# Kernel tuning notes

Measured on AMD Instinct MI355X. Metric: run time of the kernel, lower is better.

Reference implementation:

```python
import jax, jax.numpy as jnp
import numpy as np
from jax import lax

EPS = 1e-20

def _conv(x, w, b):
    # stride-2 conv, padding=1, NCHW/OIHW (torch Conv2d semantics)
    y = lax.conv_general_dilated(x, w, (2, 2), ((1, 1), (1, 1)),
                                 dimension_numbers=('NCHW', 'OIHW', 'NCHW'))
    return y + b[None, :, None, None]

def _deconv(x, w, b):
    # ConvTranspose2d(k=4, s=2, p=1): doubles spatial dims (== SAME transpose padding)
    y = lax.conv_transpose(x, w, (2, 2), 'SAME',
                           dimension_numbers=('NCHW', 'OIHW', 'NCHW'))
    return y + b[None, :, None, None]

def _enc_switch(h, win, bin_, wout, bout, wsw, bsw, gnoise):
    r = jax.nn.relu(h)
    hid = jnp.einsum('bd,kds->bks', r, win) + bin_            # [B,K,S]
    y_logits = jnp.einsum('bks,ks->bk', hid, wsw) + bsw       # [B,K]
    g = -jnp.log(gnoise + EPS)                                # Gumbel noise
    y_soft = jax.nn.softmax(y_logits + g, axis=1)
    y_index = jnp.argmax(y_soft, axis=1)                      # [B]
    one_hot = jax.nn.one_hot(y_index, y_logits.shape[1], dtype=y_soft.dtype)
    y_hard = one_hot - lax.stop_gradient(y_soft) + y_soft     # straight-through
    outs = jnp.einsum('bks,ksd->bkd', hid, wout) + bout       # [B,K,192]
    out = jnp.take_along_axis(outs, y_index[:, None, None], axis=1)[:, 0]
    gate = jnp.take_along_axis(y_hard, y_index[:, None], axis=1)  # [B,1] (training gate)
    return h + out * gate, y_logits, y_index, y_hard

def _dec_switch(h, win, bin_, wout, bout, y_index, y_hard):
    r = jax.nn.relu(h)
    hid = jnp.einsum('bd,kds->bks', r, win) + bin_
    outs = jnp.einsum('bks,ksd->bkd', hid, wout) + bout
    out = jnp.take_along_axis(outs, y_index[:, None, None], axis=1)[:, 0]
    gate = jnp.take_along_axis(y_hard, y_index[:, None], axis=1)
    return h + out * gate

def setup_inputs() -> dict:
    key = jax.random.key(0)
    B, C, L, D, K, S = 1024, 3, 10, 192, 10, 10
    ks = jax.random.split(key, 48)
    def n(i, shape, s=0.05):
        return jax.random.normal(ks[i], shape, jnp.float32) * s
    return {
        'x': jax.random.uniform(ks[0], (B, C, 64, 64), jnp.float32),
        'gnoise': jax.random.exponential(ks[1], (L, B, K)).astype(jnp.float32),
        'znoise': jax.random.normal(ks[2], (B, L), jnp.float32),
        'cw1': n(3, (32, C, 4, 4)), 'cb1': n(4, (32,)),
        'cw2': n(5, (32, 32, 4, 4)), 'cb2': n(6, (32,)),
        'cw3': n(7, (64, 32, 4, 4)), 'cb3': n(8, (64,)),
        'cw4': n(9, (64, 64, 4, 4)), 'cb4': n(10, (64,)),
        'fc_w': n(11, (1024, D)), 'fc_b': n(12, (D,)),
        'ein_w': n(13, (L, K, D, S)), 'ein_b': n(14, (L, K, S)),
        'eout_w': n(15, (L, K, S, D)), 'eout_b': n(16, (L, K, D)),
        'esw_w': n(17, (L, K, S)), 'esw_b': n(18, (L, K)),
        'mean_w': n(19, (D, L)), 'mean_b': n(20, (L,)),
        'lv_w': n(21, (D, L)), 'lv_b': n(22, (L,)),
        'fcl_w': n(23, (L, D)), 'fcl_b': n(24, (D,)),
        'din_w': n(25, (L, K, D, S)), 'din_b': n(26, (L, K, S)),
        'dout_w': n(27, (L, K, S, D)), 'dout_b': n(28, (L, K, D)),
        'dfc_w': n(29, (D, 1024)), 'dfc_b': n(30, (1024,)),
        'dw1': n(31, (64, 64, 4, 4)), 'db1': n(32, (64,)),
        'dw2': n(33, (32, 64, 4, 4)), 'db2': n(34, (32,)),
        'dw3': n(35, (32, 32, 4, 4)), 'db3': n(36, (32,)),
        'dw4': n(37, (C, 32, 4, 4)), 'db4': n(38, (C,)),
    }

def reference(x, gnoise, znoise, cw1, cb1, cw2, cb2, cw3, cb3, cw4, cb4,
              fc_w, fc_b, ein_w, ein_b, eout_w, eout_b, esw_w, esw_b,
              mean_w, mean_b, lv_w, lv_b, fcl_w, fcl_b,
              din_w, din_b, dout_w, dout_b, dfc_w, dfc_b,
              dw1, db1, dw2, db2, dw3, db3, dw4, db4):
    # ---- encoder convs ----
    h = jax.nn.relu(_conv(x, cw1, cb1))
    h = jax.nn.relu(_conv(h, cw2, cb2))
    h = jax.nn.relu(_conv(h, cw3, cb3))
    h = jax.nn.relu(_conv(h, cw4, cb4))           # [B,64,4,4]
    h = h.reshape(-1, 1024) @ fc_w + fc_b         # [B,192]
    # ---- encoder FC switches (sequential over latents) ----
    L = ein_w.shape[0]
    ys_index, ys_hard = [], []
    for i in range(L):
        h, _, yi, yh = _enc_switch(h, ein_w[i], ein_b[i], eout_w[i], eout_b[i],
                                   esw_w[i], esw_b[i], gnoise[i])
        ys_index.append(yi); ys_hard.append(yh)
    r = jax.nn.relu(h)
    z_mean = r @ mean_w + mean_b
    z_logvar = r @ lv_w + lv_b
    # ---- reparameterize ----
    z = znoise * jnp.exp(z_logvar / 2) + z_mean
    # ---- decoder ----
    d = z @ fcl_w + fcl_b
    for i in range(L):
        d = _dec_switch(d, din_w[i], din_b[i], dout_w[i], dout_b[i],
                        ys_index[i], ys_hard[i])
    d = jax.nn.relu(d)
    d = jax.nn.relu(d @ dfc_w + dfc_b)
    d = d.reshape(-1, 64, 4, 4)
    d = jax.nn.relu(_deconv(d, dw1, db1))
    d = jax.nn.relu(_deconv(d, dw2, db2))
    d = jax.nn.relu(_deconv(d, dw3, db3))
    recon_x = _deconv(d, dw4, db4)                # [B,C,64,64] logits
    return recon_x, z, z_mean, z_logvar
```

## Files before the change

kernel.cpp:

```cpp
#include <hip/hip_runtime.h>
#include <hip/hip_bf16.h>
#include <math.h>


#define BATCH 1024

using short8  = __attribute__((ext_vector_type(8))) short;
using f32x4   = __attribute__((ext_vector_type(4))) float;
using ushort4v = __attribute__((ext_vector_type(4))) ushort;

__device__ __forceinline__ ushort f2bf(float f) {
    uint u = __float_as_uint(f);
    uint r = (u + 0x7fffu + ((u >> 16) & 1u)) >> 16;
    return (ushort)r;
}
__device__ __forceinline__ float bf2f(ushort u) {
    return __uint_as_float(((uint)u) << 16);
}

__device__ __forceinline__ void conv_frag_elem(const float* __restrict__ w,
                                               ushort* __restrict__ frag,
                                               int idx, int CIN, int COUT) {
    int NCH = CIN / 32, NT = COUT / 16;
    int j = idx & 7; int lane = (idx >> 3) & 63; int rest = idx >> 9;
    int ntile = rest % NT; rest /= NT;
    int ch = rest % NCH; int tap = rest / NCH;
    int o = ntile * 16 + (lane & 15);
    int i = ch * 32 + (lane >> 4) * 8 + j;
    frag[idx] = f2bf(w[((size_t)(o * CIN + i)) * 16 + tap]);
}
__device__ __forceinline__ void deconv_frag_elem(const float* __restrict__ w,
                                                 ushort* __restrict__ frag,
                                                 int idx, int CIN, int COUT) {
    int NCH = CIN / 32, NT = COUT / 16;
    int j = idx & 7; int lane = (idx >> 3) & 63; int rest = idx >> 9;
    int ntile = rest % NT; rest /= NT;
    int ch = rest % NCH; rest /= NCH;
    int tapidx = rest % 4; int cls = rest / 4;
    int py = cls >> 1, px = cls & 1, a = tapidx >> 1, b = tapidx & 1;
    int tap = (py + 2 * a) * 4 + (px + 2 * b);
    int o = ntile * 16 + (lane & 15);
    int i = ch * 32 + (lane >> 4) * 8 + j;
    frag[idx] = f2bf(w[((size_t)(o * CIN + i)) * 16 + tap]);
}

__global__ __launch_bounds__(256)
void prep_all(const float* __restrict__ cw1, const float* __restrict__ cw2,
              const float* __restrict__ cw3, const float* __restrict__ cw4,
              const float* __restrict__ dw1, const float* __restrict__ dw2,
              const float* __restrict__ dw3, const float* __restrict__ dw4,
              const float* __restrict__ ein_w, const float* __restrict__ fc_w,
              const float* __restrict__ dfc_w, const float* __restrict__ x,
              ushort* __restrict__ c1g, ushort* __restrict__ c2g,
              ushort* __restrict__ c3g, ushort* __restrict__ c4g,
              ushort* __restrict__ d1g, ushort* __restrict__ d2g,
              ushort* __restrict__ d3g, ushort* __restrict__ d4g,
              ushort* __restrict__ encwTb, ushort* __restrict__ fc1g,
              ushort* __restrict__ dfcg, ushort* __restrict__ xh) {
    const int b = blockIdx.x, t = threadIdx.x;
    if (b < 8) {
        int idx = b * 256 + t;
        if (idx < 2048) {
            int j = idx & 7; int lane = (idx >> 3) & 63;
            int ntile = (idx >> 9) & 1; int s = idx >> 10;
            int o = ntile * 16 + (lane & 15);
            int kg = lane >> 4;
            int tap = s * 8 + kg * 2 + (j >> 2);
            int c = j & 3;
            c1g[idx] = (c < 3) ? f2bf(cw1[((size_t)(o * 3 + c)) * 16 + tap]) : (ushort)0;
        }
    } else if (b < 72) {
        conv_frag_elem(cw2, c2g, (b - 8) * 256 + t, 32, 32);
    } else if (b < 200) {
        conv_frag_elem(cw3, c3g, (b - 72) * 256 + t, 32, 64);
    } else if (b < 456) {
        conv_frag_elem(cw4, c4g, (b - 200) * 256 + t, 64, 64);
    } else if (b < 712) {
        deconv_frag_elem(dw1, d1g, (b - 456) * 256 + t, 64, 64);
    } else if (b < 840) {
        deconv_frag_elem(dw2, d2g, (b - 712) * 256 + t, 64, 32);
    } else if (b < 904) {
        deconv_frag_elem(dw3, d3g, (b - 840) * 256 + t, 32, 32);
    } else if (b < 936) {
        int idx = (b - 904) * 256 + t;
        if (idx < 4608) {
            int jj = idx & 7; int lane = (idx >> 3) & 63; int nbi = idx >> 9;
            int dy = nbi / 3, dx = nbi % 3;
            int j = lane & 15;
            int k = (lane >> 4) * 8 + jj;
            int cls = j >> 2, och = j & 3;
            int py = cls >> 1, px = cls & 1;
            int a2 = dy - py, b2 = dx - px;
            ushort v = 0;
            if (och < 3 && (unsigned)a2 < 2u && (unsigned)b2 < 2u) {
                int tap = (py + 2 * a2) * 4 + (px + 2 * b2);
                v = f2bf(dw4[((size_t)(och * 32 + k)) * 16 + tap]);
            }
            d4g[idx] = v;
        }
    } else if (b < 1686) {
        int idx = (b - 936) * 256 + t;
        if (idx < 192000) {
            int ks = idx % 100;
            int d = (idx / 100) % 192;
            int l = idx / 19200;
            int k = ks / 10, s = ks % 10;
            encwTb[idx] = f2bf(ein_w[(size_t)l * 19200 + k * 1920 + d * 10 + s]);
        }
    } else if (b < 2454) {
        int idx = (b - 1686) * 256 + t;
        int jj = idx & 7; int lane = (idx >> 3) & 63; int rest = idx >> 9;
        int nt = rest % 12, s = rest / 12;
        int k_nat = s * 32 + (lane >> 4) * 8 + jj;
        int d = (k_nat & 63) * 16 + (k_nat >> 6);
        int j = nt * 16 + (lane & 15);
        fc1g[idx] = f2bf(fc_w[(size_t)d * 192 + j]);
    } else if (b < 3222) {
        int idx = (b - 2454) * 256 + t;
        int jj = idx & 7; int lane = (idx >> 3) & 63; int rest = idx >> 9;
        int nt = rest % 64, s = rest / 64;
        int k = s * 32 + (lane >> 4) * 8 + jj;
        int j_nat = nt * 16 + (lane & 15);
        int d = (j_nat & 63) * 16 + (j_nat >> 6);
        dfcg[idx] = f2bf(dfc_w[(size_t)k * 1024 + d]);
    } else {
        const int n = b - 3222;
        const float* xb = x + (size_t)n * 12288;
        ushort* ob = xh + ((size_t)n << 14);
        #pragma unroll
        for (int i = 0; i < 4; ++i) {
            const int p0 = (i * 256 + t) << 2;
            const float4 v0 = *(const float4*)(xb + p0);
            const float4 v1 = *(const float4*)(xb + 4096 + p0);
            const float4 v2 = *(const float4*)(xb + 8192 + p0);
            short8 o0, o1;
            o0[0] = (short)f2bf(v0.x); o0[1] = (short)f2bf(v1.x); o0[2] = (short)f2bf(v2.x); o0[3] = 0;
            o0[4] = (short)f2bf(v0.y); o0[5] = (short)f2bf(v1.y); o0[6] = (short)f2bf(v2.y); o0[7] = 0;
            o1[0] = (short)f2bf(v0.z); o1[1] = (short)f2bf(v1.z); o1[2] = (short)f2bf(v2.z); o1[3] = 0;
            o1[4] = (short)f2bf(v0.w); o1[5] = (short)f2bf(v1.w); o1[6] = (short)f2bf(v2.w); o1[7] = 0;
            *(short8*)(ob + (size_t)(p0 << 2)) = o0;
            *(short8*)(ob + (size_t)(p0 << 2) + 8) = o1;
        }
    }
}

__global__ __launch_bounds__(512)
void conv12_fused(const ushort* __restrict__ xh, const ushort* __restrict__ w1frag,
                  const float* __restrict__ b1, const ushort* __restrict__ w2frag,
                  const float* __restrict__ b2, ushort* __restrict__ out) {
    __shared__ ushort mid[576 * 40];
    const int t = threadIdx.x;
    const int lane = t & 63, w = t >> 6;
    const int m = lane & 15, kg = lane >> 4;
    const int h = blockIdx.x & 1, n = blockIdx.x >> 1;
    const int base = 16 * h - 1;
    const ushort* xb = xh + ((size_t)n << 14);

    short8 bf1[4];
    #pragma unroll
    for (int f = 0; f < 4; ++f)
        bf1[f] = *(const short8*)(w1frag + (f << 9) + lane * 8);

    auto gatherA = [&](int mt, short8* av) {
        const int lp = mt * 16 + m;
        const int lx = lp & 31, lyy = lp >> 5;
        const int my = base + lyy;
        const int iy0 = 2 * my - 1, ix0 = 2 * lx - 1;
        #pragma unroll
        for (int s = 0; s < 2; ++s) {
            union { ushort4v h4[2]; short8 s8; } a;
            #pragma unroll
            for (int tt = 0; tt < 2; ++tt) {
                const int tap = s * 8 + kg * 2 + tt;
                const int ky = tap >> 2, kx = tap & 3;
                const int iy = iy0 + ky, ix = ix0 + kx;
                ushort4v v = {0, 0, 0, 0};
                if ((unsigned)iy < 64u && (unsigned)ix < 64u)
                    v = *(const ushort4v*)(xb + (size_t)(((iy << 6) + ix) << 2));
                a.h4[tt] = v;
            }
            av[s] = a.s8;
        }
    };
    auto commitA = [&](int mt, short8* av) {
        f32x4 acc[2] = {{0,0,0,0},{0,0,0,0}};
        #pragma unroll
        for (int s = 0; s < 2; ++s)
            #pragma unroll
            for (int nt = 0; nt < 2; ++nt)
                acc[nt] = __builtin_amdgcn_mfma_f32_16x16x32_bf16(av[s], bf1[s * 2 + nt], acc[nt], 0, 0, 0);
        #pragma unroll
        for (int nt = 0; nt < 2; ++nt) {
            const int och = (nt << 4) + m;
            const float bv = b1[och];
            #pragma unroll
            for (int r = 0; r < 4; ++r) {
                const int lpr = (mt << 4) + (kg << 2) + r;
                mid[(size_t)lpr * 40 + och] = f2bf(fmaxf(acc[nt][r] + bv, 0.f));
            }
        }
    };

    {
        short8 avA[2], avB[2];
        gatherA(w, avA);
        gatherA(w + 8, avB);
        commitA(w, avA);
        commitA(w + 8, avB);
        gatherA(w + 16, avA);
        gatherA(w + 24, avB);
        commitA(w + 16, avA);
        commitA(w + 24, avB);
        if (w < 4) {
            gatherA(w + 32, avA);
            commitA(w + 32, avA);
        }
    }
    __syncthreads();
    for (int it = 0; it < 2; ++it) {
        const int u = it * 8 + w;
        const int nt = u & 1, mt2 = u >> 1;
        const int p2 = (mt2 << 4) + m;
        const int ox2 = p2 & 15, ly2 = p2 >> 4;
        const int oy2 = 8 * h + ly2;
        const int iy0 = 2 * oy2 - 1, ix0 = 2 * ox2 - 1;
        f32x4 acc = {0, 0, 0, 0};
        const ushort* wl = w2frag + ((size_t)nt << 9) + lane * 8;
        #pragma unroll
        for (int ky = 0; ky < 4; ++ky) {
            const int iy = iy0 + ky;
            const bool vy = (unsigned)iy < 32u;
            const int liy = iy - base;
            #pragma unroll
            for (int kx = 0; kx < 4; ++kx) {
                const int ix = ix0 + kx;
                const bool v = vy && ((unsigned)ix < 32u);
                short8 a = {0, 0, 0, 0, 0, 0, 0, 0};
                if (v) a = *(const short8*)(mid + (size_t)((liy << 5) + ix) * 40 + kg * 8);
                const short8 b = *(const short8*)(wl + ((size_t)((ky * 4 + kx) * 2) << 9));
                acc = __builtin_amdgcn_mfma_f32_16x16x32_bf16(a, b, acc, 0, 0, 0);
            }
        }
        const int och = (nt << 4) + m;
        const float bv = b2[och];
        ushort* ob = out + ((size_t)n * 256 + 128 * h + (mt2 << 4) + (kg << 2)) * 32;
        #pragma unroll
        for (int r = 0; r < 4; ++r)
            ob[r * 32 + och] = f2bf(fmaxf(acc[r] + bv, 0.f));
    }
}

__global__ __launch_bounds__(256)
void conv34_fused(const ushort* __restrict__ in, const ushort* __restrict__ w3frag,
                  const float* __restrict__ b3, const ushort* __restrict__ w4frag,
                  const float* __restrict__ b4, ushort* __restrict__ out) {
    __shared__ ushort mid[64 * 64];
    const int t = threadIdx.x;
    const int lane = t & 63, w = t >> 6;
    const int m = lane & 15, kg = lane >> 4;
    const int n = blockIdx.x;
    const ushort* ibase = in + ((size_t)n << 13);

    {
        const int p = (w << 4) + m;
        const int ox = p & 7, oy = p >> 3;
        const int iy0 = 2 * oy - 1, ix0 = 2 * ox - 1;
        f32x4 acc[4] = {{0,0,0,0},{0,0,0,0},{0,0,0,0},{0,0,0,0}};
        #pragma unroll
        for (int ky = 0; ky < 4; ++ky) {
            const int iy = iy0 + ky;
            const bool vy = (unsigned)iy < 16u;
            #pragma unroll
            for (int kx = 0; kx < 4; ++kx) {
                const int ix = ix0 + kx;
                const bool v = vy && ((unsigned)ix < 16u);
                short8 a = {0, 0, 0, 0, 0, 0, 0, 0};
                if (v) a = *(const short8*)(ibase + (size_t)((iy << 4) + ix) * 32 + kg * 8);
                const int tap = ky * 4 + kx;
                #pragma unroll
                for (int nt = 0; nt < 4; ++nt) {
                    const short8 b = *(const short8*)(w3frag + ((size_t)(tap * 4 + nt) << 9) + lane * 8);
                    acc[nt] = __builtin_amdgcn_mfma_f32_16x16x32_bf16(a, b, acc[nt], 0, 0, 0);
                }
            }
        }
        #pragma unroll
        for (int nt = 0; nt < 4; ++nt) {
            const int och = (nt << 4) + m;
            const float bv = b3[och];
            #pragma unroll
            for (int r = 0; r < 4; ++r) {
                const int pr = (w << 4) + (kg << 2) + r;
                mid[(size_t)pr * 64 + och] = f2bf(fmaxf(acc[nt][r] + bv, 0.f));
            }
        }
    }
    __syncthreads();
    {
        const int ox = m & 3, oy = m >> 2;
        const int iy0 = 2 * oy - 1, ix0 = 2 * ox - 1;
        f32x4 acc = {0, 0, 0, 0};
        const ushort* wl = w4frag + ((size_t)w << 9) + lane * 8;
        #pragma unroll
        for (int ky = 0; ky < 4; ++ky) {
            const int iy = iy0 + ky;
            const bool vy = (unsigned)iy < 8u;
            #pragma unroll
            for (int kx = 0; kx < 4; ++kx) {
                const int ix = ix0 + kx;
                const bool v = vy && ((unsigned)ix < 8u);
                const int tap = ky * 4 + kx;
                #pragma unroll
                for (int ch = 0; ch < 2; ++ch) {
                    short8 a = {0, 0, 0, 0, 0, 0, 0, 0};
                    if (v) a = *(const short8*)(mid + (size_t)((iy << 3) + ix) * 64 + ch * 32 + kg * 8);
                    const short8 b = *(const short8*)(wl + ((size_t)((tap * 2 + ch) * 4) << 9));
                    acc = __builtin_amdgcn_mfma_f32_16x16x32_bf16(a, b, acc, 0, 0, 0);
                }
            }
        }
        const int och = (w << 4) + m;
        const float bv = b4[och];
        #pragma unroll
        for (int r = 0; r < 4; ++r)
            out[((size_t)n * 16 + (kg << 2) + r) * 64 + och] = f2bf(fmaxf(acc[r] + bv, 0.f));
    }
}

__global__ __launch_bounds__(256)
void deconv12_fused(const ushort* __restrict__ in, const ushort* __restrict__ w1frag,
                    const float* __restrict__ b1, const ushort* __restrict__ w2frag,
                    const float* __restrict__ b2, ushort* __restrict__ out) {
    __shared__ ushort mid[64 * 64];
    const int t = threadIdx.x;
    const int lane = t & 63, w = t >> 6;
    const int m = lane & 15, kg = lane >> 4;
    const int n = blockIdx.x;
    const ushort* ibase = in + ((size_t)n << 10);

    {
        const int oxh = m & 3, oyh = m >> 2;
        f32x4 acc[4] = {{0,0,0,0},{0,0,0,0},{0,0,0,0},{0,0,0,0}};
        const ushort* wl = w1frag + ((size_t)w << 9) + lane * 8;
        #pragma unroll
        for (int ch = 0; ch < 2; ++ch) {
            short8 nb[3][3];
            #pragma unroll
            for (int dy = 0; dy < 3; ++dy) {
                const int iy = oyh + dy - 1;
                const bool vy = (unsigned)iy < 4u;
                #pragma unroll
                for (int dx = 0; dx < 3; ++dx) {
                    const int ix = oxh + dx - 1;
                    short8 a = {0, 0, 0, 0, 0, 0, 0, 0};
                    if (vy && (unsigned)ix < 4u)
                        a = *(const short8*)(ibase + (size_t)((iy << 2) + ix) * 64 + ch * 32 + kg * 8);
                    nb[dy][dx] = a;
                }
            }
            #pragma unroll
            for (int cls = 0; cls < 4; ++cls) {
                const int py = cls >> 1, px = cls & 1;
                #pragma unroll
                for (int ti = 0; ti < 4; ++ti) {
                    const int a2 = ti >> 1, b2i = ti & 1;
                    const short8 b = *(const short8*)(wl + ((size_t)(((cls * 4 + ti) * 2 + ch) * 4) << 9));
                    acc[cls] = __builtin_amdgcn_mfma_f32_16x16x32_bf16(nb[py + a2][px + b2i], b, acc[cls], 0, 0, 0);
                }
            }
        }
        const int och = (w << 4) + m;
        const float bv = b1[och];
        #pragma unroll
        for (int cls = 0; cls < 4; ++cls) {
            const int py = cls >> 1, px = cls & 1;
            #pragma unroll
            for (int r = 0; r < 4; ++r) {
                const int qq = (kg << 2) + r;
                const int oxh2 = qq & 3, oyh2 = qq >> 2;
                const int oy = 2 * oyh2 + py, ox = 2 * oxh2 + px;
                mid[(size_t)((oy << 3) + ox) * 64 + och] = f2bf(fmaxf(acc[cls][r] + bv, 0.f));
            }
        }
    }
    __syncthreads();
    for (int u = w; u < 8; u += 4) {
        const int nt = u & 1, mt = u >> 1;
        const int q = (mt << 4) + m;
        const int oxh = q & 7, oyh = q >> 3;
        f32x4 acc[4] = {{0,0,0,0},{0,0,0,0},{0,0,0,0},{0,0,0,0}};
        const ushort* wl = w2frag + ((size_t)nt << 9) + lane * 8;
        #pragma unroll
        for (int ch = 0; ch < 2; ++ch) {
            short8 nb[3][3];
            #pragma unroll
            for (int dy = 0; dy < 3; ++dy) {
                const int iy = oyh + dy - 1;
                const bool vy = (unsigned)iy < 8u;
                #pragma unroll
                for (int dx = 0; dx < 3; ++dx) {
                    const int ix = oxh + dx - 1;
                    short8 a = {0, 0, 0, 0, 0, 0, 0, 0};
                    if (vy && (unsigned)ix < 8u)
                        a = *(const short8*)(mid + (size_t)((iy << 3) + ix) * 64 + ch * 32 + kg * 8);
                    nb[dy][dx] = a;
                }
            }
            #pragma unroll
            for (int cls = 0; cls < 4; ++cls) {
                const int py = cls >> 1, px = cls & 1;
                #pragma unroll
                for (int ti = 0; ti < 4; ++ti) {
                    const int a2 = ti >> 1, b2i = ti & 1;
                    const short8 b = *(const short8*)(wl + ((size_t)(((cls * 4 + ti) * 2 + ch) * 2) << 9));
                    acc[cls] = __builtin_amdgcn_mfma_f32_16x16x32_bf16(nb[py + a2][px + b2i], b, acc[cls], 0, 0, 0);
                }
            }
        }
        const int och = (nt << 4) + m;
        const float bv = b2[och];
        #pragma unroll
        for (int cls = 0; cls < 4; ++cls) {
            const int py = cls >> 1, px = cls & 1;
            #pragma unroll
            for (int r = 0; r < 4; ++r) {
                const int qq = (mt << 4) + (kg << 2) + r;
                const int oxh2 = qq & 7, oyh2 = qq >> 3;
                const int oy = 2 * oyh2 + py, ox = 2 * oxh2 + px;
                out[((size_t)(n * 16 + oy) * 16 + ox) * 32 + och] = f2bf(fmaxf(acc[cls][r] + bv, 0.f));
            }
        }
    }
}

__global__ __launch_bounds__(256)
void deconv34_fused(const ushort* __restrict__ in, const ushort* __restrict__ w3frag,
                    const float* __restrict__ b3, const ushort* __restrict__ w4frag,
                    const float* __restrict__ b4, float* __restrict__ out) {
    __shared__ ushort mid[20 * 32 * 32];
    const int t = threadIdx.x;
    const int lane = t & 63, w = t >> 6;
    const int m = lane & 15, kg = lane >> 4;
    const int h = blockIdx.x & 1, n = blockIdx.x >> 1;
    const int base = 16 * h - 2;
    const ushort* ibase = in + ((size_t)n << 13);

    for (int u = w; u < 20; u += 4) {
        const int nt = u & 1, mt = u >> 1;
        const int ir = 8 * h - 1 + mt;
        short8 nb[3][3];
        #pragma unroll
        for (int dy = 0; dy < 3; ++dy) {
            const int iy = ir + dy - 1;
            const bool vy = (unsigned)iy < 16u;
            #pragma unroll
            for (int dx = 0; dx < 3; ++dx) {
                const int ix = m + dx - 1;
                short8 a = {0, 0, 0, 0, 0, 0, 0, 0};
                if (vy && (unsigned)ix < 16u)
                    a = *(const short8*)(ibase + (size_t)((iy << 4) + ix) * 32 + kg * 8);
                nb[dy][dx] = a;
            }
        }
        const ushort* wl = w3frag + ((size_t)nt << 9) + lane * 8;
        f32x4 acc[4] = {{0,0,0,0},{0,0,0,0},{0,0,0,0},{0,0,0,0}};
        #pragma unroll
        for (int cls = 0; cls < 4; ++cls) {
            const int py = cls >> 1, px = cls & 1;
            #pragma unroll
            for (int ti = 0; ti < 4; ++ti) {
                const int a2 = ti >> 1, b2 = ti & 1;
                const short8 b = *(const short8*)(wl + ((size_t)((cls * 4 + ti) * 2) << 9));
                acc[cls] = __builtin_amdgcn_mfma_f32_16x16x32_bf16(nb[py + a2][px + b2], b, acc[cls], 0, 0, 0);
            }
        }
        const int och = (nt << 4) + m;
        const int ochSw = och ^ (kg << 3);
        const float bv = b3[och];
        #pragma unroll
        for (int cls = 0; cls < 4; ++cls) {
            const int py = cls >> 1, px = cls & 1;
            const int ly = 2 * mt + py;
            #pragma unroll
            for (int r = 0; r < 4; ++r) {
                const int ox = ((kg << 3) + 2 * r) + px;
                mid[(size_t)((ly << 5) + ox) * 32 + ochSw] = f2bf(fmaxf(acc[cls][r] + bv, 0.f));
            }
        }
    }
    __syncthreads();
    const int clsB = m >> 2, ochB = m & 3;
    const int pyB = clsB >> 1, pxB = clsB & 1;
    for (int it = 0; it < 8; ++it) {
        const int mt2 = it * 4 + w;
        const int oyh = 16 * h + (mt2 >> 1);
        const int oxh = ((mt2 & 1) << 4) + m;
        short8 nb[3][3];
        #pragma unroll
        for (int dy = 0; dy < 3; ++dy) {
            const int iy = oyh + dy - 1;
            const bool vy = (unsigned)iy < 32u;
            const int ly = iy - base;
            #pragma unroll
            for (int dx = 0; dx < 3; ++dx) {
                const int ix = oxh + dx - 1;
                short8 a = {0, 0, 0, 0, 0, 0, 0, 0};
                if (vy && (unsigned)ix < 32u) {
                    const int rb = (kg ^ ((ix >> 3) & 3)) << 3;
                    a = *(const short8*)(mid + (size_t)((ly << 5) + ix) * 32 + rb);
                }
                nb[dy][dx] = a;
            }
        }
        f32x4 acc = {0, 0, 0, 0};
        const ushort* wl = w4frag + lane * 8;
        #pragma unroll
        for (int dy = 0; dy < 3; ++dy)
            #pragma unroll
            for (int dx = 0; dx < 3; ++dx) {
                const short8 b = *(const short8*)(wl + ((size_t)(dy * 3 + dx) << 9));
                acc = __builtin_amdgcn_mfma_f32_16x16x32_bf16(nb[dy][dx], b, acc, 0, 0, 0);
            }
        if (ochB < 3) {
            const float bv = b4[ochB];
            float* ob = out + (size_t)n * 12288 + ochB * 4096;
            const int oy = 2 * oyh + pyB;
            #pragma unroll
            for (int r = 0; r < 4; ++r) {
                const int xp = ((mt2 & 1) << 4) + (kg << 2) + r;
                ob[oy * 64 + 2 * xp + pxB] = acc[r] + bv;
            }
        }
    }
}

__global__ __launch_bounds__(256)
void fc1_mfma(const ushort* __restrict__ in, const ushort* __restrict__ frag,
              const float* __restrict__ bias, float* __restrict__ out) {
    const int lane = threadIdx.x & 63;
    const int gw = (blockIdx.x << 2) + (threadIdx.x >> 6);
    const int nt = gw % 12, mt = gw / 12;
    const int m = lane & 15, kg = lane >> 4;
    const ushort* arow = in + ((size_t)(mt * 16 + m) << 10) + kg * 8;
    const ushort* wl = frag + nt * 512 + lane * 8;
    f32x4 acc0 = {0, 0, 0, 0}, acc1 = {0, 0, 0, 0};
    #pragma unroll
    for (int s = 0; s < 32; s += 2) {
        const short8 a0 = *(const short8*)(arow + s * 32);
        const short8 a1 = *(const short8*)(arow + s * 32 + 32);
        const short8 b0 = *(const short8*)(wl + ((size_t)(s * 12) << 9));
        const short8 b1 = *(const short8*)(wl + ((size_t)((s + 1) * 12) << 9));
        acc0 = __builtin_amdgcn_mfma_f32_16x16x32_bf16(a0, b0, acc0, 0, 0, 0);
        acc1 = __builtin_amdgcn_mfma_f32_16x16x32_bf16(a1, b1, acc1, 0, 0, 0);
    }
    const int j = nt * 16 + m;
    const float bv = bias[j];
    #pragma unroll
    for (int r = 0; r < 4; ++r)
        out[(size_t)(mt * 16 + kg * 4 + r) * 192 + j] = (acc0[r] + acc1[r]) + bv;
}

__global__ __launch_bounds__(256)
void dfc_mfma(const ushort* __restrict__ in, const ushort* __restrict__ frag,
              const float* __restrict__ bias, ushort* __restrict__ out) {
    const int lane = threadIdx.x & 63;
    const int gw = (blockIdx.x << 2) + (threadIdx.x >> 6);
    const int ntg = gw & 15, mt = gw >> 4;
    const int m = lane & 15, kg = lane >> 4;
    const ushort* arow = in + (size_t)(mt * 16 + m) * 192 + kg * 8;
    const ushort* wl = frag + ((size_t)(ntg * 4) << 9) + lane * 8;
    f32x4 acc[4] = {{0,0,0,0},{0,0,0,0},{0,0,0,0},{0,0,0,0}};
    #pragma unroll
    for (int s = 0; s < 6; ++s) {
        const short8 a = *(const short8*)(arow + s * 32);
        #pragma unroll
        for (int q = 0; q < 4; ++q) {
            const short8 b = *(const short8*)(wl + ((size_t)(s * 64 + q) << 9));
            acc[q] = __builtin_amdgcn_mfma_f32_16x16x32_bf16(a, b, acc[q], 0, 0, 0);
        }
    }
    #pragma unroll
    for (int q = 0; q < 4; ++q) {
        const int j_nat = (ntg * 4 + q) * 16 + m;
        const int d = (j_nat & 63) * 16 + (j_nat >> 6);
        const float bv = bias[d];
        #pragma unroll
        for (int r = 0; r < 4; ++r) {
            const float vv = fmaxf(acc[q][r] + bv, 0.f);
            out[((size_t)(mt * 16 + kg * 4 + r) << 10) + j_nat] = f2bf(vv);
        }
    }
}

__global__ __launch_bounds__(256)
void enc_switch4(float* __restrict__ h,
                 const ushort* __restrict__ winTb,
                 const float* __restrict__ bin_all,
                 const float* __restrict__ wout_all,
                 const float* __restrict__ bout_all,
                 const float* __restrict__ wsw_all,
                 const float* __restrict__ bsw_all,
                 const float* __restrict__ gn_all,
                 int* __restrict__ yidx, float* __restrict__ gateArr) {
    const int t = threadIdx.x;
    const int b0 = blockIdx.x << 2;
    __shared__ float hold[4][192], r[4][192], part[4][200], hid[4][100], lg[4][10];
    __shared__ int yi_s[4]; __shared__ float gate_s[4];
    if (t < 192) {
        #pragma unroll
        for (int row = 0; row < 4; ++row) {
            const float v = h[(size_t)(b0 + row) * 192 + t];
            hold[row][t] = v; r[row][t] = fmaxf(v, 0.f);
        }
    }
    for (int i = 0; i < 10; ++i) {
        __syncthreads();
        if (t < 200) {
            const int ks = (t < 100) ? t : t - 100;
            const int half = (t < 100) ? 0 : 1;
            const ushort* wp = winTb + (size_t)i * 19200 + (half * 96) * 100 + ks;
            const float* r0 = &r[0][half * 96];
            const float* r1 = &r[1][half * 96];
            const float* r2 = &r[2][half * 96];
            const float* r3 = &r[3][half * 96];
            float a0 = 0.f, a1 = 0.f, a2 = 0.f, a3 = 0.f;
            #pragma unroll
            for (int dd = 0; dd < 96; ++dd) {
                const float wv = bf2f(wp[dd * 100]);
                a0 = fmaf(r0[dd], wv, a0);
                a1 = fmaf(r1[dd], wv, a1);
                a2 = fmaf(r2[dd], wv, a2);
                a3 = fmaf(r3[dd], wv, a3);
            }
            part[0][t] = a0; part[1][t] = a1; part[2][t] = a2; part[3][t] = a3;
        }
        __syncthreads();
        if (t < 100) {
            const float bv = bin_all[i * 100 + t];
            #pragma unroll
            for (int row = 0; row < 4; ++row)
                hid[row][t] = part[row][t] + part[row][t + 100] + bv;
        }
        __syncthreads();
        if (t < 40) {
            const int row = t / 10, k = t % 10;
            const float* wsw = wsw_all + i * 100 + k * 10;
            float acc = bsw_all[i * 10 + k];
            #pragma unroll
            for (int s = 0; s < 10; ++s) acc = fmaf(hid[row][k * 10 + s], wsw[s], acc);
            lg[row][k] = acc - logf(gn_all[(size_t)i * 10240 + (b0 + row) * 10 + k] + 1e-20f);
        }
        __syncthreads();
        if (t < 4) {
            int bi = 0; float best = lg[t][0];
            #pragma unroll
            for (int k = 1; k < 10; ++k) if (lg[t][k] > best) { best = lg[t][k]; bi = k; }
            float sum = 0.f;
            #pragma unroll
            for (int k = 0; k < 10; ++k) sum += expf(lg[t][k] - best);
            const float ysoft = 1.0f / sum;
            yi_s[t] = bi;
            const float g = (1.0f - ysoft) + ysoft;
            gate_s[t] = g;
            yidx[i * 1024 + b0 + t] = bi;
            gateArr[i * 1024 + b0 + t] = g;
        }
        __syncthreads();
        if (t < 192) {
            #pragma unroll
            for (int row = 0; row < 4; ++row) {
                const int yi = yi_s[row];
                const float gate = gate_s[row];
                const float* wb = wout_all + (size_t)i * 19200 + yi * 1920 + t;
                float acc = bout_all[i * 1920 + yi * 192 + t];
                #pragma unroll
                for (int s = 0; s < 10; ++s) acc = fmaf(hid[row][yi * 10 + s], wb[s * 192], acc);
                const float nv = hold[row][t] + acc * gate;
                hold[row][t] = nv; r[row][t] = fmaxf(nv, 0.f);
            }
        }
    }
    __syncthreads();
    if (t < 192) {
        #pragma unroll
        for (int row = 0; row < 4; ++row)
            h[(size_t)(b0 + row) * 192 + t] = hold[row][t];
    }
}

__global__ __launch_bounds__(256)
void dec_switch_all(const float* __restrict__ h,
                    const float* __restrict__ win_all,
                    const float* __restrict__ bin_all,
                    const float* __restrict__ wout_all,
                    const float* __restrict__ bout_all,
                    const int* __restrict__ yidx, const float* __restrict__ gateArr,
                    ushort* __restrict__ dbf) {
    const int b = blockIdx.x, t = threadIdx.x;
    __shared__ float hold[192], r[192], part[240], hid[10];
    if (t < 192) { float v = h[(size_t)b * 192 + t]; hold[t] = v; r[t] = fmaxf(v, 0.f); }
    for (int i = 0; i < 10; ++i) {
        const int yi = yidx[i * 1024 + b];
        const float gate = gateArr[i * 1024 + b];
        __syncthreads();
        if (t < 240) {
            const int s = t % 10, g = t / 10;
            const float* wp = win_all + (size_t)i * 19200 + yi * 1920 + s;
            const int d0 = g * 8;
            float a0 = 0.f, a1 = 0.f;
            #pragma unroll
            for (int dd = 0; dd < 8; dd += 2) {
                a0 = fmaf(r[d0 + dd + 0], wp[(d0 + dd + 0) * 10], a0);
                a1 = fmaf(r[d0 + dd + 1], wp[(d0 + dd + 1) * 10], a1);
            }
            part[t] = a0 + a1;
        }
        __syncthreads();
        if (t < 10) {
            float acc = bin_all[i * 100 + yi * 10 + t];
            #pragma unroll
            for (int g = 0; g < 24; ++g) acc += part[g * 10 + t];
            hid[t] = acc;
        }
        __syncthreads();
        if (t < 192) {
            const float* wp = wout_all + (size_t)i * 19200 + yi * 1920 + t;
            float acc = bout_all[i * 1920 + yi * 192 + t];
            #pragma unroll
            for (int s = 0; s < 10; ++s) acc = fmaf(hid[s], wp[s * 192], acc);
            float nv = hold[t] + acc * gate;
            hold[t] = nv; r[t] = fmaxf(nv, 0.f);
        }
    }
    if (t < 192) dbf[(size_t)b * 192 + t] = f2bf(r[t]);
}

__global__ __launch_bounds__(192)
void zfcl_kernel(const float* __restrict__ h,
                 const float* __restrict__ mw, const float* __restrict__ mb,
                 const float* __restrict__ lw, const float* __restrict__ lb,
                 const float* __restrict__ zn,
                 const float* __restrict__ fw, const float* __restrict__ fb,
                 float* __restrict__ out_z, float* __restrict__ out_mean,
                 float* __restrict__ out_lv, float* __restrict__ dbuf) {
    const int b = blockIdx.x, t = threadIdx.x;
    __shared__ float r[192], pm[160], pl[160], zsh[10];
    for (int d = t; d < 192; d += 192) r[d] = fmaxf(h[(size_t)b * 192 + d], 0.f);
    __syncthreads();
    if (t < 160) {
        const int l = t % 10, g = t / 10;
        float am = 0.f, al = 0.f;
        #pragma unroll
        for (int d = g * 12; d < g * 12 + 12; ++d) {
            am = fmaf(r[d], mw[d * 10 + l], am);
            al = fmaf(r[d], lw[d * 10 + l], al);
        }
        pm[t] = am; pl[t] = al;
    }
    __syncthreads();
    if (t < 10) {
        float zm = mb[t], zl = lb[t];
        #pragma unroll
        for (int g = 0; g < 16; ++g) { zm += pm[g * 10 + t]; zl += pl[g * 10 + t]; }
        const float z = zn[(size_t)b * 10 + t] * expf(zl * 0.5f) + zm;
        out_mean[(size_t)b * 10 + t] = zm;
        out_lv[(size_t)b * 10 + t] = zl;
        out_z[(size_t)b * 10 + t] = z;
        zsh[t] = z;
    }
    __syncthreads();
    for (int d = t; d < 192; d += 192) {
        float acc = fb[d];
        #pragma unroll
        for (int l = 0; l < 10; ++l) acc = fmaf(zsh[l], fw[l * 192 + d], acc);
        dbuf[(size_t)b * 192 + d] = acc;
    }
}

extern "C" void kernel_launch(void* const* d_in, const int* in_sizes, int n_in,
                              void* d_out, int out_size, void* d_ws, size_t ws_size,
                              hipStream_t stream) {
    const float* x      = (const float*)d_in[0];
    const float* gnoise = (const float*)d_in[1];
    const float* znoise = (const float*)d_in[2];
    const float* cw1 = (const float*)d_in[3];  const float* cb1 = (const float*)d_in[4];
    const float* cw2 = (const float*)d_in[5];  const float* cb2 = (const float*)d_in[6];
    const float* cw3 = (const float*)d_in[7];  const float* cb3 = (const float*)d_in[8];
    const float* cw4 = (const float*)d_in[9];  const float* cb4 = (const float*)d_in[10];
    const float* fc_w = (const float*)d_in[11]; const float* fc_b = (const float*)d_in[12];
    const float* ein_w = (const float*)d_in[13]; const float* ein_b = (const float*)d_in[14];
    const float* eout_w = (const float*)d_in[15]; const float* eout_b = (const float*)d_in[16];
    const float* esw_w = (const float*)d_in[17]; const float* esw_b = (const float*)d_in[18];
    const float* mean_w = (const float*)d_in[19]; const float* mean_b = (const float*)d_in[20];
    const float* lv_w = (const float*)d_in[21]; const float* lv_b = (const float*)d_in[22];
    const float* fcl_w = (const float*)d_in[23]; const float* fcl_b = (const float*)d_in[24];
    const float* din_w = (const float*)d_in[25]; const float* din_b = (const float*)d_in[26];
    const float* dout_w = (const float*)d_in[27]; const float* dout_b = (const float*)d_in[28];
    const float* dfc_w = (const float*)d_in[29]; const float* dfc_b = (const float*)d_in[30];
    const float* dw1 = (const float*)d_in[31]; const float* db1 = (const float*)d_in[32];
    const float* dw2 = (const float*)d_in[33]; const float* db2 = (const float*)d_in[34];
    const float* dw3 = (const float*)d_in[35]; const float* db3 = (const float*)d_in[36];
    const float* dw4 = (const float*)d_in[37]; const float* db4 = (const float*)d_in[38];

    float* out = (float*)d_out;
    float* recon  = out;
    float* z_out  = out + 12582912;
    float* zm_out = z_out + 10240;
    float* zl_out = zm_out + 10240;

    char* ws = (char*)d_ws;
    ushort* xh    = (ushort*)(ws);
    ushort* bufB  = (ushort*)(ws + 100663296);
    ushort* bufD  = (ushort*)(ws + 125829120);
    float*  bufH  = (float*) (ws + 127926272);
    float*  bufD2 = (float*) (ws + 128712704);
    int*    yidx  = (int*)   (ws + 129499136);
    float*  gate  = (float*) (ws + 129540096);
    char*   fb    = ws + 129581056;
    ushort* c1g = (ushort*)(fb);
    ushort* c2g = (ushort*)(fb + 4096);
    ushort* c3g = (ushort*)(fb + 36864);
    ushort* c4g = (ushort*)(fb + 102400);
    ushort* d1g = (ushort*)(fb + 233472);
    ushort* d2g = (ushort*)(fb + 364544);
    ushort* d3g = (ushort*)(fb + 430080);
    ushort* d4g = (ushort*)(fb + 462848);
    ushort* encwTb = (ushort*)(fb + 479232);
    ushort* fc1g  = (ushort*)(fb + 1247232);
    ushort* dfcg  = (ushort*)(fb + 1640448);
    ushort* dbf   = (ushort*)(fb + 2033664);

    prep_all<<<4246, 256, 0, stream>>>(cw1, cw2, cw3, cw4, dw1, dw2, dw3, dw4,
                                       ein_w, fc_w, dfc_w, x,
                                       c1g, c2g, c3g, c4g, d1g, d2g, d3g, d4g,
                                       encwTb, fc1g, dfcg, xh);

    conv12_fused<<<2048, 512, 0, stream>>>(xh, c1g, cb1, c2g, cb2, bufB);
    conv34_fused<<<1024, 256, 0, stream>>>(bufB, c3g, cb3, c4g, cb4, bufD);
    fc1_mfma<<<192, 256, 0, stream>>>(bufD, fc1g, fc_b, bufH);
    enc_switch4<<<256, 256, 0, stream>>>(bufH, encwTb, ein_b, eout_w, eout_b,
                                         esw_w, esw_b, gnoise, yidx, gate);
    zfcl_kernel<<<1024, 192, 0, stream>>>(bufH, mean_w, mean_b, lv_w, lv_b,
                                          znoise, fcl_w, fcl_b,
                                          z_out, zm_out, zl_out, bufD2);
    dec_switch_all<<<1024, 256, 0, stream>>>(bufD2, din_w, din_b, dout_w, dout_b,
                                             yidx, gate, dbf);
    dfc_mfma<<<256, 256, 0, stream>>>(dbf, dfcg, dfc_b, bufD);

    deconv12_fused<<<1024, 256, 0, stream>>>(bufD, d1g, db1, d2g, db2, bufB);
    deconv34_fused<<<2048, 256, 0, stream>>>(bufB, d3g, db3, d4g, db4, recon);
}
```

Baseline: 220.4 us.

## Map one wavefront per batch row in encoder and decoder switch kernels

Both switch kernels are restructured so each 64-lane wavefront handles one batch row and keeps its running hidden state in registers. This removes the block-wide __syncthreads between stages. The decoder kernel now packs 4 rows per block on a quarter of the previous grid. The trade-off is long serial reduction loops on a few lanes (50 lanes over 192 inputs, or 10 lanes in the decoder) with less weight sharing across rows. It also relies on implicit wavefront lockstep for shared-memory visibility between lanes.

```diff
diff --git a/kernel.cpp b/kernel.cpp
--- a/kernel.cpp
+++ b/kernel.cpp
@@ -603,89 +603,65 @@
                  const float* __restrict__ gn_all,
                  int* __restrict__ yidx, float* __restrict__ gateArr) {
     const int t = threadIdx.x;
-    const int b0 = blockIdx.x << 2;
-    __shared__ float hold[4][192], r[4][192], part[4][200], hid[4][100], lg[4][10];
-    __shared__ int yi_s[4]; __shared__ float gate_s[4];
-    if (t < 192) {
-        #pragma unroll
-        for (int row = 0; row < 4; ++row) {
-            const float v = h[(size_t)(b0 + row) * 192 + t];
-            hold[row][t] = v; r[row][t] = fmaxf(v, 0.f);
-        }
+    const int lane = t & 63, row = t >> 6;
+    const int b = (blockIdx.x << 2) + row;
+    __shared__ float r_s[4][192], hid_s[4][100], lg_s[4][10];
+    float hold0[3];
+    #pragma unroll
+    for (int q = 0; q < 3; ++q) {
+        const int d = (q << 6) + lane;
+        const float v = h[(size_t)b * 192 + d];
+        hold0[q] = v; r_s[row][d] = fmaxf(v, 0.f);
     }
     for (int i = 0; i < 10; ++i) {
-        __syncthreads();
-        if (t < 200) {
-            const int ks = (t < 100) ? t : t - 100;
-            const int half = (t < 100) ? 0 : 1;
-            const ushort* wp = winTb + (size_t)i * 19200 + (half * 96) * 100 + ks;
-            const float* r0 = &r[0][half * 96];
-            const float* r1 = &r[1][half * 96];
-            const float* r2 = &r[2][half * 96];
-            const float* r3 = &r[3][half * 96];
-            float a0 = 0.f, a1 = 0.f, a2 = 0.f, a3 = 0.f;
-            #pragma unroll
-            for (int dd = 0; dd < 96; ++dd) {
-                const float wv = bf2f(wp[dd * 100]);
-                a0 = fmaf(r0[dd], wv, a0);
-                a1 = fmaf(r1[dd], wv, a1);
-                a2 = fmaf(r2[dd], wv, a2);
-                a3 = fmaf(r3[dd], wv, a3);
-            }
-            part[0][t] = a0; part[1][t] = a1; part[2][t] = a2; part[3][t] = a3;
-        }
-        __syncthreads();
-        if (t < 100) {
-            const float bv = bin_all[i * 100 + t];
-            #pragma unroll
-            for (int row = 0; row < 4; ++row)
-                hid[row][t] = part[row][t] + part[row][t + 100] + bv;
-        }
-        __syncthreads();
-        if (t < 40) {
-            const int row = t / 10, k = t % 10;
-            const float* wsw = wsw_all + i * 100 + k * 10;
-            float acc = bsw_all[i * 10 + k];
-            #pragma unroll
-            for (int s = 0; s < 10; ++s) acc = fmaf(hid[row][k * 10 + s], wsw[s], acc);
-            lg[row][k] = acc - logf(gn_all[(size_t)i * 10240 + (b0 + row) * 10 + k] + 1e-20f);
-        }
-        __syncthreads();
-        if (t < 4) {
-            int bi = 0; float best = lg[t][0];
-            #pragma unroll
-            for (int k = 1; k < 10; ++k) if (lg[t][k] > best) { best = lg[t][k]; bi = k; }
-            float sum = 0.f;
-            #pragma unroll
-            for (int k = 0; k < 10; ++k) sum += expf(lg[t][k] - best);
-            const float ysoft = 1.0f / sum;
-            yi_s[t] = bi;
-            const float g = (1.0f - ysoft) + ysoft;
-            gate_s[t] = g;
-            yidx[i * 1024 + b0 + t] = bi;
-            gateArr[i * 1024 + b0 + t] = g;
-        }
-        __syncthreads();
-        if (t < 192) {
-            #pragma unroll
-            for (int row = 0; row < 4; ++row) {
-                const int yi = yi_s[row];
-                const float gate = gate_s[row];
-                const float* wb = wout_all + (size_t)i * 19200 + yi * 1920 + t;
-                float acc = bout_all[i * 1920 + yi * 192 + t];
-                #pragma unroll
-                for (int s = 0; s < 10; ++s) acc = fmaf(hid[row][yi * 10 + s], wb[s * 192], acc);
-                const float nv = hold[row][t] + acc * gate;
-                hold[row][t] = nv; r[row][t] = fmaxf(nv, 0.f);
-            }
-        }
-    }
-    __syncthreads();
-    if (t < 192) {
-        #pragma unroll
-        for (int row = 0; row < 4; ++row)
-            h[(size_t)(b0 + row) * 192 + t] = hold[row][t];
-    }
+        if (lane < 50) {
+            const ushort* wp = winTb + (size_t)i * 19200 + lane * 2;
+            float a0 = bin_all[i * 100 + lane * 2];
+            float a1 = bin_all[i * 100 + lane * 2 + 1];
+            #pragma unroll 4
+            for (int d = 0; d < 192; ++d) {
+                const float rv = r_s[row][d];
+                const uint wv = *(const uint*)(wp + d * 100);
+                a0 = fmaf(rv, bf2f((ushort)wv), a0);
+                a1 = fmaf(rv, bf2f((ushort)(wv >> 16)), a1);
+            }
+            hid_s[row][lane * 2] = a0;
+            hid_s[row][lane * 2 + 1] = a1;
+        }
+        if (lane < 10) {
+            const float* wsw = wsw_all + i * 100 + lane * 10;
+            float acc = bsw_all[i * 10 + lane];
+            #pragma unroll
+            for (int s = 0; s < 10; ++s) acc = fmaf(hid_s[row][lane * 10 + s], wsw[s], acc);
+            lg_s[row][lane] = acc - logf(gn_all[(size_t)i * 10240 + b * 10 + lane] + 1e-20f);
+        }
+        int bi = 0; float best = lg_s[row][0];
+        #pragma unroll
+        for (int k = 1; k < 10; ++k) {
+            const float v = lg_s[row][k];
+            if (v > best) { best = v; bi = k; }
+        }
+        float sum = 0.f;
+        #pragma unroll
+        for (int k = 0; k < 10; ++k) sum += expf(lg_s[row][k] - best);
+        const float ysoft = 1.0f / sum;
+        const float g = (1.0f - ysoft) + ysoft;
+        if (lane == 0) { yidx[i * 1024 + b] = bi; gateArr[i * 1024 + b] = g; }
+        const float* wb = wout_all + (size_t)i * 19200 + bi * 1920;
+        const float* bo = bout_all + i * 1920 + bi * 192;
+        #pragma unroll
+        for (int q = 0; q < 3; ++q) {
+            const int d = (q << 6) + lane;
+            float acc = bo[d];
+            #pragma unroll
+            for (int s = 0; s < 10; ++s) acc = fmaf(hid_s[row][bi * 10 + s], wb[s * 192 + d], acc);
+            const float nv = hold0[q] + acc * g;
+            hold0[q] = nv; r_s[row][d] = fmaxf(nv, 0.f);
+        }
+    }
+    #pragma unroll
+    for (int q = 0; q < 3; ++q)
+        h[(size_t)b * 192 + (q << 6) + lane] = hold0[q];
 }
 
 __global__ __launch_bounds__(256)
@@ -696,43 +672,45 @@
                     const float* __restrict__ bout_all,
                     const int* __restrict__ yidx, const float* __restrict__ gateArr,
                     ushort* __restrict__ dbf) {
-    const int b = blockIdx.x, t = threadIdx.x;
-    __shared__ float hold[192], r[192], part[240], hid[10];
-    if (t < 192) { float v = h[(size_t)b * 192 + t]; hold[t] = v; r[t] = fmaxf(v, 0.f); }
+    const int t = threadIdx.x;
+    const int lane = t & 63, row = t >> 6;
+    const int b = (blockIdx.x << 2) + row;
+    __shared__ float r_s[4][192], hid_s[4][10];
+    float hold0[3];
+    #pragma unroll
+    for (int q = 0; q < 3; ++q) {
+        const int d = (q << 6) + lane;
+        const float v = h[(size_t)b * 192 + d];
+        hold0[q] = v; r_s[row][d] = fmaxf(v, 0.f);
+    }
     for (int i = 0; i < 10; ++i) {
         const int yi = yidx[i * 1024 + b];
         const float gate = gateArr[i * 1024 + b];
-        __syncthreads();
-        if (t < 240) {
-            const int s = t % 10, g = t / 10;
-            const float* wp = win_all + (size_t)i * 19200 + yi * 1920 + s;
-            const int d0 = g * 8;
-            float a0 = 0.f, a1 = 0.f;
-            #pragma unroll
-            for (int dd = 0; dd < 8; dd += 2) {
-                a0 = fmaf(r[d0 + dd + 0], wp[(d0 + dd + 0) * 10], a0);
-                a1 = fmaf(r[d0 + dd + 1], wp[(d0 + dd + 1) * 10], a1);
-            }
-            part[t] = a0 + a1;
-        }
-        __syncthreads();
-        if (t < 10) {
-            float acc = bin_all[i * 100 + yi * 10 + t];
-            #pragma unroll
-            for (int g = 0; g < 24; ++g) acc += part[g * 10 + t];
-            hid[t] = acc;
-        }
-        __syncthreads();
-        if (t < 192) {
-            const float* wp = wout_all + (size_t)i * 19200 + yi * 1920 + t;
-            float acc = bout_all[i * 1920 + yi * 192 + t];
-            #pragma unroll
-            for (int s = 0; s < 10; ++s) acc = fmaf(hid[s], wp[s * 192], acc);
-            float nv = hold[t] + acc * gate;
-            hold[t] = nv; r[t] = fmaxf(nv, 0.f);
-        }
-    }
-    if (t < 192) dbf[(size_t)b * 192 + t] = f2bf(r[t]);
+        if (lane < 10) {
+            const float* wp = win_all + (size_t)i * 19200 + yi * 1920 + lane;
+            float a0 = bin_all[i * 100 + yi * 10 + lane], a1 = 0.f;
+            #pragma unroll 4
+            for (int d = 0; d < 192; d += 2) {
+                a0 = fmaf(r_s[row][d], wp[d * 10], a0);
+                a1 = fmaf(r_s[row][d + 1], wp[(d + 1) * 10], a1);
+            }
+            hid_s[row][lane] = a0 + a1;
+        }
+        const float* wb = wout_all + (size_t)i * 19200 + yi * 1920;
+        const float* bo = bout_all + i * 1920 + yi * 192;
+        #pragma unroll
+        for (int q = 0; q < 3; ++q) {
+            const int d = (q << 6) + lane;
+            float acc = bo[d];
+            #pragma unroll
+            for (int s = 0; s < 10; ++s) acc = fmaf(hid_s[row][s], wb[s * 192 + d], acc);
+            const float nv = hold0[q] + acc * gate;
+            hold0[q] = nv; r_s[row][d] = fmaxf(nv, 0.f);
+        }
+    }
+    #pragma unroll
+    for (int q = 0; q < 3; ++q)
+        dbf[(size_t)b * 192 + (q << 6) + lane] = f2bf(fmaxf(hold0[q], 0.f));
 }
 
 __global__ __launch_bounds__(192)
@@ -843,8 +821,8 @@
     zfcl_kernel<<<1024, 192, 0, stream>>>(bufH, mean_w, mean_b, lv_w, lv_b,
                                           znoise, fcl_w, fcl_b,
                                           z_out, zm_out, zl_out, bufD2);
-    dec_switch_all<<<1024, 256, 0, stream>>>(bufD2, din_w, din_b, dout_w, dout_b,
-                                             yidx, gate, dbf);
+    dec_switch_all<<<256, 256, 0, stream>>>(bufD2, din_w, din_b, dout_w, dout_b,
+                                            yidx, gate, dbf);
     dfc_mfma<<<256, 256, 0, stream>>>(dbf, dfcg, dfc_b, bufD);
 
     deconv12_fused<<<1024, 256, 0, stream>>>(bufD, d1g, db1, d2g, db2, bufB);
```

New measurement: 370.4 us. 1.68x slower.
